# Optimization experiments

Measured on AMD Instinct MI355X. Metric: run time of the kernel, lower is better.

Reference implementation:

```python
import jax, jax.numpy as jnp
import numpy as np

VOCAB_SIZE = 128
MEMORY_SLOTS = 2048
READ_K = 8


def _build_memory(enc_hidden, num_pairs, memory_slots):
    # Round-robin circular-buffer write, vectorized: the final content of slot s
    # is enc_hidden[:, p] where p is the LAST position < L with p % M == s.
    B, T, H = enc_hidden.shape
    L = min(num_pairs * 2, T - 3)  # num_pairs is a Python int -> static
    slots = np.arange(memory_slots)
    last_pos = slots + memory_slots * ((L - 1 - slots) // memory_slots)
    valid = slots < L  # slots never written stay zero
    last_pos = np.where(valid, np.clip(last_pos, 0, T - 1), 0)
    gathered = enc_hidden[:, jnp.asarray(last_pos), :]          # (B, M, H)
    mask = jnp.asarray(valid, enc_hidden.dtype)[None, :, None]  # (1, M, 1)
    return gathered * mask


def _k_sparse_softmax(raw, k):
    # softmax over only the top-k scores; all other probs are exactly 0
    B, N = raw.shape
    topk_vals, topk_idx = jax.lax.top_k(raw, k)          # (B, k)
    probs = jax.nn.softmax(topk_vals, axis=-1)           # (B, k)
    attn = jnp.zeros_like(raw)
    attn = attn.at[jnp.arange(B)[:, None], topk_idx].set(probs)
    return attn


def setup_inputs() -> dict:
    key = jax.random.key(0)
    ks = jax.random.split(key, 5)
    B, T, H = 32, 4096, 512
    return {
        "enc_hidden": jax.random.normal(ks[0], (B, T, H), jnp.float32),
        "query_hidden": jax.random.normal(ks[1], (B, H), jnp.float32),
        "num_pairs": 2000,
        "q_w": jax.random.normal(ks[2], (H, H), jnp.float32) * 0.02,
        "q_b": jnp.zeros((H,), jnp.float32),
        "k_w": jax.random.normal(ks[3], (H, H), jnp.float32) * 0.02,
        "k_b": jnp.zeros((H,), jnp.float32),
        "out_w": jax.random.normal(ks[4], (H, VOCAB_SIZE), jnp.float32) * 0.02,
        "out_b": jnp.zeros((VOCAB_SIZE,), jnp.float32),
    }


def reference(enc_hidden, query_hidden, num_pairs, q_w, q_b, k_w, k_b, out_w, out_b):
    B, T, H = enc_hidden.shape
    memory = _build_memory(enc_hidden, num_pairs, MEMORY_SLOTS)  # (B, M, H)
    q = query_hidden @ q_w + q_b                                 # (B, H)
    k = memory @ k_w + k_b                                       # (B, M, H)
    raw = jnp.einsum("bh,bmh->bm", q, k) / (H ** 0.5)          # (B, M)
    attn = _k_sparse_softmax(raw, READ_K)                        # (B, M)
    retrieved = jnp.einsum("bm,bmh->bh", attn, memory)          # (B, H)
    logits = (retrieved + query_hidden) @ out_w + out_b          # (B, VOCAB)
    return logits
```

## Files before the change

kernel.cpp:

```cpp
#include <hip/hip_runtime.h>
#include <math.h>

#define BB 32
#define TT 4096
#define HH 512
#define MM 2048
#define VV 128
#define KK 8

#define INV_SQRT_H 0.044194173824159216f

__global__ __launch_bounds__(512) void qproj_kernel(
    const float* __restrict__ query, const float* __restrict__ q_w,
    const float* __restrict__ q_b, float* __restrict__ q) {
  int b = blockIdx.x, j = threadIdx.x;
  __shared__ __align__(16) float qs[HH];
  qs[j] = query[b * HH + j];
  __syncthreads();
  float acc = q_b[j];
#pragma unroll 8
  for (int h = 0; h < HH; ++h) acc = fmaf(qs[h], q_w[h * HH + j], acc);
  q[b * HH + j] = acc;
}

__global__ __launch_bounds__(512) void kproj_kernel(
    const float* __restrict__ q, const float* __restrict__ k_w,
    const float* __restrict__ k_b, float* __restrict__ qk,
    float* __restrict__ qb_dot) {
  int b = blockIdx.x, tid = threadIdx.x;
  int lane = tid & 63, wave = tid >> 6;
  __shared__ __align__(16) float qs[HH];
  qs[tid] = q[b * HH + tid];
  __syncthreads();
  const float4* qr = (const float4*)qs;
  for (int h = wave; h < HH; h += 8) {
    const float4* kr = (const float4*)(k_w + (size_t)h * HH);
    float4 a0 = kr[lane], a1 = kr[lane + 64];
    float4 b0 = qr[lane], b1 = qr[lane + 64];
    float acc = a0.x * b0.x + a0.y * b0.y + a0.z * b0.z + a0.w * b0.w +
                a1.x * b1.x + a1.y * b1.y + a1.z * b1.z + a1.w * b1.w;
#pragma unroll
    for (int off = 32; off; off >>= 1) acc += __shfl_down(acc, off);
    if (lane == 0) qk[b * HH + h] = acc;
  }
  if (wave == 0) {
    float acc = 0.f;
    for (int j = lane; j < HH; j += 64) acc = fmaf(qs[j], k_b[j], acc);
#pragma unroll
    for (int off = 32; off; off >>= 1) acc += __shfl_down(acc, off);
    if (lane == 0) qb_dot[b] = acc;
  }
}

__global__ __launch_bounds__(256) void score_kernel(
    const float* __restrict__ enc, const float* __restrict__ qk,
    const float* __restrict__ qb_dot, const int* __restrict__ num_pairs,
    float* __restrict__ scores) {
  int gw = (blockIdx.x * 256 + threadIdx.x) >> 6;
  int lane = threadIdx.x & 63;
  int b = gw >> 11;
  int m = gw & (MM - 1);
  int L = min(2 * num_pairs[0], TT - 3);
  float qbd = qb_dot[b];
  float s;
  if (m < L) {
    int p = m + MM * ((L - 1 - m) / MM);
    const float4* row = (const float4*)(enc + ((size_t)b * TT + p) * HH);
    const float4* qr = (const float4*)(qk + (size_t)b * HH);
    float4 a0 = row[lane], a1 = row[lane + 64];
    float4 b0 = qr[lane], b1 = qr[lane + 64];
    float acc = a0.x * b0.x + a0.y * b0.y + a0.z * b0.z + a0.w * b0.w +
                a1.x * b1.x + a1.y * b1.y + a1.z * b1.z + a1.w * b1.w;
#pragma unroll
    for (int off = 32; off; off >>= 1) acc += __shfl_down(acc, off);
    s = (acc + qbd) * INV_SQRT_H;
  } else {
    s = qbd * INV_SQRT_H;
  }
  if (lane == 0) scores[b * MM + m] = s;
}

__global__ __launch_bounds__(256) void finalize_kernel(
    const float* __restrict__ enc, const float* __restrict__ scores,
    const float* __restrict__ query, const float* __restrict__ out_w,
    const float* __restrict__ out_b, const int* __restrict__ num_pairs,
    float* __restrict__ out) {
  int b = blockIdx.x, tid = threadIdx.x;
  __shared__ float sv[MM];
  __shared__ float rv[256];
  __shared__ int ri[256];
  __shared__ float topv[KK];
  __shared__ int topi[KK];
  __shared__ float rq[HH];

  for (int i = tid; i < MM; i += 256) sv[i] = scores[b * MM + i];
  __syncthreads();

  for (int k = 0; k < KK; ++k) {
    float best = -INFINITY;
    int bi = 0x7FFFFFFF;
    for (int i = tid; i < MM; i += 256) {
      float v = sv[i];
      if (v > best) { best = v; bi = i; }
    }
    rv[tid] = best;
    ri[tid] = bi;
    __syncthreads();
    for (int s = 128; s; s >>= 1) {
      if (tid < s) {
        float ov = rv[tid + s];
        int oi = ri[tid + s];
        if (ov > rv[tid] || (ov == rv[tid] && oi < ri[tid])) {
          rv[tid] = ov;
          ri[tid] = oi;
        }
      }
      __syncthreads();
    }
    if (tid == 0) {
      topv[k] = rv[0];
      topi[k] = ri[0];
      sv[ri[0]] = -INFINITY;
    }
    __syncthreads();
  }

  float mx = topv[0];
#pragma unroll
  for (int k = 1; k < KK; ++k) mx = fmaxf(mx, topv[k]);
  float p[KK];
  float se = 0.f;
#pragma unroll
  for (int k = 0; k < KK; ++k) { p[k] = expf(topv[k] - mx); se += p[k]; }
  float inv = 1.f / se;

  int L = min(2 * num_pairs[0], TT - 3);
  for (int h = tid; h < HH; h += 256) {
    float acc = query[b * HH + h];
#pragma unroll
    for (int k = 0; k < KK; ++k) {
      int m = topi[k];
      if (m < L) {
        int pp = m + MM * ((L - 1 - m) / MM);
        acc = fmaf(p[k] * inv, enc[((size_t)b * TT + pp) * HH + h], acc);
      }
    }
    rq[h] = acc;
  }
  __syncthreads();

  if (tid < VV) {
    float acc = out_b[tid];
#pragma unroll 8
    for (int h = 0; h < HH; ++h) acc = fmaf(rq[h], out_w[h * VV + tid], acc);
    out[b * VV + tid] = acc;
  }
}

extern "C" void kernel_launch(void* const* d_in, const int* in_sizes, int n_in,
                              void* d_out, int out_size, void* d_ws,
                              size_t ws_size, hipStream_t stream) {
  const float* enc = (const float*)d_in[0];
  const float* query = (const float*)d_in[1];
  const int* num_pairs = (const int*)d_in[2];
  const float* q_w = (const float*)d_in[3];
  const float* q_b = (const float*)d_in[4];
  const float* k_w = (const float*)d_in[5];
  const float* k_b = (const float*)d_in[6];
  const float* out_w = (const float*)d_in[7];
  const float* out_b = (const float*)d_in[8];
  float* out = (float*)d_out;

  char* ws = (char*)d_ws;
  float* q = (float*)(ws);
  float* qk = (float*)(ws + 65536);
  float* qbd = (float*)(ws + 131072);
  float* scores = (float*)(ws + 132096);

  hipLaunchKernelGGL(qproj_kernel, dim3(BB), dim3(HH), 0, stream,
                     query, q_w, q_b, q);
  hipLaunchKernelGGL(kproj_kernel, dim3(BB), dim3(HH), 0, stream,
                     q, k_w, k_b, qk, qbd);
  hipLaunchKernelGGL(score_kernel, dim3(BB * MM / 4), dim3(256), 0, stream,
                     enc, qk, qbd, num_pairs, scores);
  hipLaunchKernelGGL(finalize_kernel, dim3(BB), dim3(256), 0, stream,
                     enc, scores, query, out_w, out_b, num_pairs, out);
}
```

Measured before the change: 451.8 us.

## Fuse query and key projections into one kernel; do top-k in a single wave

Merges the q projection and k_w·q projection into one kernel so the projected query stays in shared memory instead of being written to and reloaded from the workspace, which also removes one launch. The finalize kernel's top-k now runs in a single wavefront that holds all 2048 scores in registers and reduces with shuffles, replacing eight rounds of block-wide shared-memory reductions and barriers. The selected positions and softmax weights are precomputed once by lane 0. The costs are high register use in wave 0 (32 scores plus the top-k state) and the other waves sitting idle during selection.

```diff
diff --git a/kernel.cpp b/kernel.cpp
--- a/kernel.cpp
+++ b/kernel.cpp
@@ -10,45 +10,40 @@
 
 #define INV_SQRT_H 0.044194173824159216f
 
-__global__ __launch_bounds__(512) void qproj_kernel(
+__global__ __launch_bounds__(512) void qk_kernel(
     const float* __restrict__ query, const float* __restrict__ q_w,
-    const float* __restrict__ q_b, float* __restrict__ q) {
-  int b = blockIdx.x, j = threadIdx.x;
-  __shared__ __align__(16) float qs[HH];
-  qs[j] = query[b * HH + j];
-  __syncthreads();
-  float acc = q_b[j];
-#pragma unroll 8
-  for (int h = 0; h < HH; ++h) acc = fmaf(qs[h], q_w[h * HH + j], acc);
-  q[b * HH + j] = acc;
-}
-
-__global__ __launch_bounds__(512) void kproj_kernel(
-    const float* __restrict__ q, const float* __restrict__ k_w,
+    const float* __restrict__ q_b, const float* __restrict__ k_w,
     const float* __restrict__ k_b, float* __restrict__ qk,
     float* __restrict__ qb_dot) {
   int b = blockIdx.x, tid = threadIdx.x;
   int lane = tid & 63, wave = tid >> 6;
   __shared__ __align__(16) float qs[HH];
-  qs[tid] = q[b * HH + tid];
+  __shared__ __align__(16) float qv[HH];
+  qs[tid] = query[b * HH + tid];
   __syncthreads();
-  const float4* qr = (const float4*)qs;
+  float acc = q_b[tid];
+#pragma unroll 8
+  for (int h = 0; h < HH; ++h) acc = fmaf(qs[h], q_w[h * HH + tid], acc);
+  qv[tid] = acc;
+  __syncthreads();
+
+  const float4* qr = (const float4*)qv;
+  float4 b0 = qr[lane], b1 = qr[lane + 64];
   for (int h = wave; h < HH; h += 8) {
     const float4* kr = (const float4*)(k_w + (size_t)h * HH);
     float4 a0 = kr[lane], a1 = kr[lane + 64];
-    float4 b0 = qr[lane], b1 = qr[lane + 64];
-    float acc = a0.x * b0.x + a0.y * b0.y + a0.z * b0.z + a0.w * b0.w +
-                a1.x * b1.x + a1.y * b1.y + a1.z * b1.z + a1.w * b1.w;
+    float d = a0.x * b0.x + a0.y * b0.y + a0.z * b0.z + a0.w * b0.w +
+              a1.x * b1.x + a1.y * b1.y + a1.z * b1.z + a1.w * b1.w;
 #pragma unroll
-    for (int off = 32; off; off >>= 1) acc += __shfl_down(acc, off);
-    if (lane == 0) qk[b * HH + h] = acc;
+    for (int off = 32; off; off >>= 1) d += __shfl_down(d, off);
+    if (lane == 0) qk[b * HH + h] = d;
   }
   if (wave == 0) {
-    float acc = 0.f;
-    for (int j = lane; j < HH; j += 64) acc = fmaf(qs[j], k_b[j], acc);
+    float d = 0.f;
+    for (int j = lane; j < HH; j += 64) d = fmaf(qv[j], k_b[j], d);
 #pragma unroll
-    for (int off = 32; off; off >>= 1) acc += __shfl_down(acc, off);
-    if (lane == 0) qb_dot[b] = acc;
+    for (int off = 32; off; off >>= 1) d += __shfl_down(d, off);
+    if (lane == 0) qb_dot[b] = d;
   }
 }
 
@@ -86,64 +81,72 @@
     const float* __restrict__ out_b, const int* __restrict__ num_pairs,
     float* __restrict__ out) {
   int b = blockIdx.x, tid = threadIdx.x;
-  __shared__ float sv[MM];
-  __shared__ float rv[256];
-  __shared__ int ri[256];
-  __shared__ float topv[KK];
-  __shared__ int topi[KK];
-  __shared__ float rq[HH];
+  int lane = tid & 63, wave = tid >> 6;
+  __shared__ float pk[KK];
+  __shared__ int pos[KK];
+  __shared__ __align__(16) float rq[HH];
 
-  for (int i = tid; i < MM; i += 256) sv[i] = scores[b * MM + i];
+  int L = min(2 * num_pairs[0], TT - 3);
+
+  if (wave == 0) {
+    const float* srow = scores + (size_t)b * MM;
+    float v[32];
+#pragma unroll
+    for (int i = 0; i < 32; ++i) v[i] = srow[lane + 64 * i];
+
+    float topv[KK];
+    int topi[KK];
+#pragma unroll
+    for (int k = 0; k < KK; ++k) {
+      float best = -INFINITY;
+      int bi = 0x7FFFFFFF;
+#pragma unroll
+      for (int i = 0; i < 32; ++i) {
+        float x = v[i];
+        if (x > best) { best = x; bi = lane + 64 * i; }
+      }
+#pragma unroll
+      for (int off = 32; off; off >>= 1) {
+        float ov = __shfl_down(best, off);
+        int oi = __shfl_down(bi, off);
+        if (ov > best || (ov == best && oi < bi)) { best = ov; bi = oi; }
+      }
+      best = __shfl(best, 0);
+      bi = __shfl(bi, 0);
+      topv[k] = best;
+      topi[k] = bi;
+      int my = ((bi & 63) == lane) ? (bi >> 6) : -1;
+#pragma unroll
+      for (int i = 0; i < 32; ++i)
+        if (i == my) v[i] = -INFINITY;
+    }
+
+    float mx = topv[0];
+#pragma unroll
+    for (int k = 1; k < KK; ++k) mx = fmaxf(mx, topv[k]);
+    float p[KK];
+    float se = 0.f;
+#pragma unroll
+    for (int k = 0; k < KK; ++k) { p[k] = expf(topv[k] - mx); se += p[k]; }
+    float inv = 1.f / se;
+    if (lane == 0) {
+#pragma unroll
+      for (int k = 0; k < KK; ++k) {
+        pk[k] = p[k] * inv;
+        int m = topi[k];
+        pos[k] = (m < L) ? (m + MM * ((L - 1 - m) / MM)) : -1;
+      }
+    }
+  }
   __syncthreads();
 
-  for (int k = 0; k < KK; ++k) {
-    float best = -INFINITY;
-    int bi = 0x7FFFFFFF;
-    for (int i = tid; i < MM; i += 256) {
-      float v = sv[i];
-      if (v > best) { best = v; bi = i; }
-    }
-    rv[tid] = best;
-    ri[tid] = bi;
-    __syncthreads();
-    for (int s = 128; s; s >>= 1) {
-      if (tid < s) {
-        float ov = rv[tid + s];
-        int oi = ri[tid + s];
-        if (ov > rv[tid] || (ov == rv[tid] && oi < ri[tid])) {
-          rv[tid] = ov;
-          ri[tid] = oi;
-        }
-      }
-      __syncthreads();
-    }
-    if (tid == 0) {
-      topv[k] = rv[0];
-      topi[k] = ri[0];
-      sv[ri[0]] = -INFINITY;
-    }
-    __syncthreads();
-  }
-
-  float mx = topv[0];
-#pragma unroll
-  for (int k = 1; k < KK; ++k) mx = fmaxf(mx, topv[k]);
-  float p[KK];
-  float se = 0.f;
-#pragma unroll
-  for (int k = 0; k < KK; ++k) { p[k] = expf(topv[k] - mx); se += p[k]; }
-  float inv = 1.f / se;
-
-  int L = min(2 * num_pairs[0], TT - 3);
   for (int h = tid; h < HH; h += 256) {
     float acc = query[b * HH + h];
 #pragma unroll
     for (int k = 0; k < KK; ++k) {
-      int m = topi[k];
-      if (m < L) {
-        int pp = m + MM * ((L - 1 - m) / MM);
-        acc = fmaf(p[k] * inv, enc[((size_t)b * TT + pp) * HH + h], acc);
-      }
+      int pp = pos[k];
+      if (pp >= 0)
+        acc = fmaf(pk[k], enc[((size_t)b * TT + pp) * HH + h], acc);
     }
     rq[h] = acc;
   }
@@ -172,15 +175,12 @@
   float* out = (float*)d_out;
 
   char* ws = (char*)d_ws;
-  float* q = (float*)(ws);
-  float* qk = (float*)(ws + 65536);
-  float* qbd = (float*)(ws + 131072);
-  float* scores = (float*)(ws + 132096);
+  float* qk = (float*)(ws);
+  float* qbd = (float*)(ws + 65536);
+  float* scores = (float*)(ws + 66560);
 
-  hipLaunchKernelGGL(qproj_kernel, dim3(BB), dim3(HH), 0, stream,
-                     query, q_w, q_b, q);
-  hipLaunchKernelGGL(kproj_kernel, dim3(BB), dim3(HH), 0, stream,
-                     q, k_w, k_b, qk, qbd);
+  hipLaunchKernelGGL(qk_kernel, dim3(BB), dim3(HH), 0, stream,
+                     query, q_w, q_b, k_w, k_b, qk, qbd);
   hipLaunchKernelGGL(score_kernel, dim3(BB * MM / 4), dim3(256), 0, stream,
                      enc, qk, qbd, num_pairs, scores);
   hipLaunchKernelGGL(finalize_kernel, dim3(BB), dim3(256), 0, stream,
```

Result: no change. 449.7 us (-0.5%).
